# Optimization experiments

Measured on AMD Instinct MI355X. Metric: run time of the kernel, lower is better.

Reference implementation:

```python
import jax, jax.numpy as jnp
from jax import lax
import numpy as np

B, S, T, I, H, O = 128, 144, 50, 10, 64, 1


def setup_inputs() -> dict:
    key = jax.random.key(0)
    ks = jax.random.split(key, 11)
    sI = 1.0 / np.sqrt(H)
    x = jax.random.normal(ks[0], (B, S, T, I), dtype=jnp.float32)
    # PyTorch nn.GRU weights per direction: W_ih [3H,I], W_hh [3H,H], b_ih [3H], b_hh [3H]
    Wih_f = jax.random.normal(ks[1], (T, 3 * H, I), dtype=jnp.float32) * sI
    Whh_f = jax.random.normal(ks[2], (T, 3 * H, H), dtype=jnp.float32) * sI
    bih_f = jax.random.normal(ks[3], (T, 3 * H), dtype=jnp.float32) * sI
    bhh_f = jax.random.normal(ks[4], (T, 3 * H), dtype=jnp.float32) * sI
    Wih_b = jax.random.normal(ks[5], (T, 3 * H, I), dtype=jnp.float32) * sI
    Whh_b = jax.random.normal(ks[6], (T, 3 * H, H), dtype=jnp.float32) * sI
    bih_b = jax.random.normal(ks[7], (T, 3 * H), dtype=jnp.float32) * sI
    bhh_b = jax.random.normal(ks[8], (T, 3 * H), dtype=jnp.float32) * sI
    Wfc = jax.random.normal(ks[9], (T, O, 2 * H), dtype=jnp.float32) * sI
    bfc = jax.random.normal(ks[10], (T, O), dtype=jnp.float32) * sI
    return {"x": x, "Wih_f": Wih_f, "Whh_f": Whh_f, "bih_f": bih_f, "bhh_f": bhh_f,
            "Wih_b": Wih_b, "Whh_b": Whh_b, "bih_b": bih_b, "bhh_b": bhh_b,
            "Wfc": Wfc, "bfc": bfc}


def _gru_cell(x_t, h, Wih, Whh, bih, bhh):
    # PyTorch GRU cell math
    gi = x_t @ Wih.T + bih          # [B, 3H]
    gh = h @ Whh.T + bhh            # [B, 3H]
    i_r, i_z, i_n = jnp.split(gi, 3, axis=-1)
    h_r, h_z, h_n = jnp.split(gh, 3, axis=-1)
    r = jax.nn.sigmoid(i_r + h_r)
    z = jax.nn.sigmoid(i_z + h_z)
    n = jnp.tanh(i_n + r * h_n)
    return (1.0 - z) * n + z * h


def _per_turbine(xt, wih_f, whh_f, bih_f, bhh_f, wih_b, whh_b, bih_b, bhh_b, wfc, bfc):
    # xt: [B, S, I]
    x_sbi = jnp.transpose(xt, (1, 0, 2))  # [S, B, I]
    h0 = jnp.zeros((xt.shape[0], H), xt.dtype)

    def step(h, x_t):
        h = _gru_cell(x_t, h, wih_f, whh_f, bih_f, bhh_f)
        return h, None

    hf, _ = lax.scan(step, h0, x_sbi)  # forward final hidden = fwd output at t=S-1
    # backward-direction output at last timestep = first step of the reverse scan
    hb = _gru_cell(xt[:, -1, :], h0, wih_b, whh_b, bih_b, bhh_b)
    h = jnp.concatenate([hf, hb], axis=-1)  # [B, 2H]; dropout is identity at inference
    return h @ wfc.T + bfc  # [B, O]


def reference(x, Wih_f, Whh_f, bih_f, bhh_f, Wih_b, Whh_b, bih_b, bhh_b, Wfc, bfc):
    x_tbsi = jnp.transpose(x, (2, 0, 1, 3))  # [T, B, S, I]
    out = jax.vmap(_per_turbine)(x_tbsi, Wih_f, Whh_f, bih_f, bhh_f,
                                 Wih_b, Whh_b, bih_b, bhh_b, Wfc, bfc)  # [T, B, O]
    return jnp.transpose(out, (1, 2, 0))  # [B, O, T]
```

## Files before the change

kernel.cpp:

```cpp
#include <hip/hip_runtime.h>


typedef _Float16 f16;
typedef _Float16 f16x8 __attribute__((ext_vector_type(8)));
typedef float    f32x4 __attribute__((ext_vector_type(4)));

constexpr int B_N = 128, S_N = 144, T_N = 50, I_N = 10, H_N = 64, G3 = 192;
constexpr int BT16 = 16, NB16 = B_N / BT16;
constexpr int HST = 88;
constexpr float L2E = 1.44269504089f;

#define MFMA16(a, b, c) __builtin_amdgcn_mfma_f32_16x16x32_f16((a), (b), (c), 0, 0, 0)

__device__ __forceinline__ float fsig(float v) {
    return __builtin_amdgcn_rcpf(1.0f + __builtin_amdgcn_exp2f(-L2E * v));
}
__device__ __forceinline__ float ftanh(float v) {
    return 1.0f - 2.0f * __builtin_amdgcn_rcpf(1.0f + __builtin_amdgcn_exp2f(2.0f * L2E * v));
}

__global__ __launch_bounds__(256)
void pack_x(const float* __restrict__ x, f16* __restrict__ xP) {
    const int idx = blockIdx.x * 256 + threadIdx.x;
    if (idx >= B_N * S_N * T_N) return;
    const float* s = x + (size_t)idx * I_N;
    f16x8 lo, hi;
    #pragma unroll
    for (int e = 0; e < 8; ++e) lo[e] = (f16)s[e];
    hi[0] = (f16)s[8]; hi[1] = (f16)s[9]; hi[2] = (f16)1.0f;
    #pragma unroll
    for (int e = 3; e < 8; ++e) hi[e] = (f16)0.0f;
    f16* d = xP + (size_t)idx * 16;
    *(f16x8*)d = lo; *(f16x8*)(d + 8) = hi;
}

#define STEPP(ss, xf)                                                             \
    {                                                                             \
        const int cur = (ss) & 1, nxt = cur ^ 1;                                  \
        const f16x8 xA = xf;                                                      \
        if ((ss) + 2 < S_N && lg < 2)                                             \
            xf = *(const f16x8*)(xProw + (size_t)((ss) + 2) * (T_N * 16) + lg * 8); \
        const f16* hrow = &hL[tile][cur][lc][0];                                  \
        const f16x8 hA0 = *(const f16x8*)(hrow + lg * 8);                         \
        const f16x8 hA1 = *(const f16x8*)(hrow + 32 + lg * 8);                    \
        f32x4 aR  = {0,0,0,0}, aZ = {0,0,0,0}, aNH = {0,0,0,0}, aNX = {0,0,0,0};  \
        aR  = MFMA16(xA,  BxR,  aR);                                              \
        aZ  = MFMA16(xA,  BxZ,  aZ);                                              \
        aNX = MFMA16(xA,  BxN,  aNX);                                             \
        aR  = MFMA16(hA0, BhR0, aR);                                              \
        aR  = MFMA16(hA1, BhR1, aR);                                              \
        aZ  = MFMA16(hA0, BhZ0, aZ);                                              \
        aZ  = MFMA16(hA1, BhZ1, aZ);                                              \
        aNH = MFMA16(hA0, BhN0, aNH);                                             \
        aNH = MFMA16(hA1, BhN1, aNH);                                             \
        const int r0 = lg * 4;                                                    \
        _Pragma("unroll")                                                         \
        for (int j = 0; j < 4; ++j) {                                             \
            const float eA = __builtin_amdgcn_exp2f(aR[j]);                       \
            const float rr = __builtin_amdgcn_rcpf(1.0f + eA);                    \
            const float eB = __builtin_amdgcn_exp2f(aZ[j]);                       \
            const float eC = __builtin_amdgcn_exp2f(fmaf(rr, aNH[j] + bnhs, aNX[j])); \
            const float v  = 1.0f + eC;                                           \
            const float ip = __builtin_amdgcn_rcpf(v * (1.0f + eB));              \
            const float p  = (eC - 1.0f) * eB;                                    \
            ho[j] = fmaf(ho[j], v, p) * ip;                                       \
            hL[tile][nxt][r0 + j][uc + lc] = (f16)ho[j];                          \
        }                                                                         \
        asm volatile("s_waitcnt lgkmcnt(0)" ::: "memory");                        \
        __builtin_amdgcn_s_barrier();                                             \
        asm volatile("" ::: "memory");                                            \
    }

__global__ __launch_bounds__(512, 1)
void gru_pair(const f16* __restrict__ xP, const float* __restrict__ x,
              const float* __restrict__ Wih_f, const float* __restrict__ Whh_f,
              const float* __restrict__ bih_f, const float* __restrict__ bhh_f,
              const float* __restrict__ Wih_b, const float* __restrict__ bih_b,
              const float* __restrict__ bhh_b,
              const float* __restrict__ Wfc,   const float* __restrict__ bfc,
              float* __restrict__ out)
{
    __shared__ f16   hL[2][2][BT16][HST];
    __shared__ float hfL[2 * BT16][H_N + 1];
    __shared__ float hbL[2 * BT16][H_N + 1];

    const int tid  = threadIdx.x;
    const int w    = tid >> 6, l = tid & 63;
    const int tile = w >> 2;
    const int uc   = (w & 3) * 16;
    const int lc   = l & 15;
    const int lg   = l >> 4;
    const int t    = blockIdx.x >> 2;
    const int b0   = (blockIdx.x & 3) * 32 + tile * 16;

    {
        f16* hp = &hL[0][0][0][0];
        for (int i = tid; i < 2 * 2 * BT16 * HST; i += 512) hp[i] = (f16)0.0f;
    }

    const float* Whh = Whh_f + (size_t)t * G3 * H_N;
    const float* Wih = Wih_f + (size_t)t * G3 * I_N;
    const f16* xProw = xP + ((size_t)(b0 + lc) * S_N * T_N + t) * 16;

    const float sRZ = -L2E, sN = 2.0f * L2E;
    auto loadBh = [&](int g, int kk, float sc) -> f16x8 {
        const float4* p = (const float4*)(Whh + (size_t)g * H_N + kk * 32 + lg * 8);
        const float4 a = p[0], b = p[1];
        f16x8 v;
        v[0] = (f16)(sc * a.x); v[1] = (f16)(sc * a.y); v[2] = (f16)(sc * a.z); v[3] = (f16)(sc * a.w);
        v[4] = (f16)(sc * b.x); v[5] = (f16)(sc * b.y); v[6] = (f16)(sc * b.z); v[7] = (f16)(sc * b.w);
        return v;
    };
    auto loadBx = [&](int g, bool rz, float sc) -> f16x8 {
        f16x8 v;
        #pragma unroll
        for (int j = 0; j < 8; ++j) {
            const int k = lg * 8 + j;
            float val = 0.0f;
            if (k < I_N)       val = Wih[(size_t)g * I_N + k];
            else if (k == 10)  val = bih_f[t * G3 + g] + (rz ? bhh_f[t * G3 + g] : 0.0f);
            v[j] = (f16)(sc * val);
        }
        return v;
    };

    const f16x8 BhR0 = loadBh(uc + lc, 0, sRZ),        BhR1 = loadBh(uc + lc, 1, sRZ);
    const f16x8 BhZ0 = loadBh(64 + uc + lc, 0, sRZ),   BhZ1 = loadBh(64 + uc + lc, 1, sRZ);
    const f16x8 BhN0 = loadBh(128 + uc + lc, 0, sN),   BhN1 = loadBh(128 + uc + lc, 1, sN);
    const f16x8 BxR  = loadBx(uc + lc, true, sRZ);
    const f16x8 BxZ  = loadBx(64 + uc + lc, true, sRZ);
    const f16x8 BxN  = loadBx(128 + uc + lc, false, sN);
    const float bnhs = sN * bhh_f[t * G3 + 128 + uc + lc];

    f16x8 xsA, xsB;
    #pragma unroll
    for (int e = 0; e < 8; ++e) { xsA[e] = (f16)0.0f; xsB[e] = (f16)0.0f; }
    if (lg < 2) {
        xsA = *(const f16x8*)(xProw + lg * 8);
        xsB = *(const f16x8*)(xProw + (size_t)(T_N * 16) + lg * 8);
    }

    float ho[4] = {0.f, 0.f, 0.f, 0.f};

    __syncthreads();

    for (int s = 0; s < S_N; s += 2) {
        STEPP(s,     xsA)
        STEPP(s + 1, xsB)
    }

    {
        const int r0 = lg * 4;
        #pragma unroll
        for (int j = 0; j < 4; ++j) hfL[tile * BT16 + r0 + j][uc + lc] = ho[j];
    }

    {
        const int row2 = tid >> 4;
        const int j0   = (tid & 15) * 4;
        const int bq   = (blockIdx.x & 3) * 32;
        const float* wib = Wih_b + (size_t)t * G3 * I_N;
        const float* bib = bih_b + t * G3;
        const float* bhb = bhh_b + t * G3;
        float2 xr[5];
        const float2* xp2 = (const float2*)(x + (((size_t)(bq + row2) * S_N + (S_N - 1)) * T_N + t) * I_N);
        #pragma unroll
        for (int k = 0; k < 5; ++k) xr[k] = xp2[k];
        #pragma unroll
        for (int m = 0; m < 4; ++m) {
            const int j = j0 + m;
            float ir = bib[j], iz = bib[64 + j], inn = bib[128 + j];
            const float2* wr = (const float2*)(wib + (size_t)j * I_N);
            const float2* wz = (const float2*)(wib + (size_t)(64 + j) * I_N);
            const float2* wn = (const float2*)(wib + (size_t)(128 + j) * I_N);
            #pragma unroll
            for (int k = 0; k < 5; ++k) {
                ir  = fmaf(wr[k].x, xr[k].x, fmaf(wr[k].y, xr[k].y, ir));
                iz  = fmaf(wz[k].x, xr[k].x, fmaf(wz[k].y, xr[k].y, iz));
                inn = fmaf(wn[k].x, xr[k].x, fmaf(wn[k].y, xr[k].y, inn));
            }
            const float r  = fsig(ir + bhb[j]);
            const float z  = fsig(iz + bhb[64 + j]);
            const float nn = ftanh(inn + r * bhb[128 + j]);
            hbL[row2][j] = (1.0f - z) * nn;
        }
    }
    __syncthreads();

    if (tid < 2 * BT16) {
        const int bq = (blockIdx.x & 3) * 32;
        const float* wfc = Wfc + (size_t)t * 2 * H_N;
        float acc = bfc[t];
        #pragma unroll 4
        for (int j = 0; j < H_N; ++j) acc += hfL[tid][j] * wfc[j];
        #pragma unroll 4
        for (int j = 0; j < H_N; ++j) acc += hbL[tid][j] * wfc[64 + j];
        out[(size_t)(bq + tid) * T_N + t] = acc;
    }
}


#define LOADX_R(ss, q0, q1, q2, q3, q4)                                           \
    if ((ss) < S_N) {                                                             \
        const float* _p = x + (((size_t)(b0 + lc) * S_N + (ss)) * T_N + t) * I_N; \
        if (lg == 0) {                                                            \
            q0 = *(const float2*)(_p);     q1 = *(const float2*)(_p + 2);         \
            q2 = *(const float2*)(_p + 4); q3 = *(const float2*)(_p + 6);         \
        } else if (lg == 1) {                                                     \
            q4 = *(const float2*)(_p + 8);                                        \
        }                                                                         \
    }

#define STEP1(ss, q0, q1, q2, q3, q4)                                             \
    {                                                                             \
        const int cur = (ss) & 1, nxt = cur ^ 1;                                  \
        const f16* hrow = &hL[cur][lc][0];                                        \
        const f16x8 hA0 = *(const f16x8*)(hrow + lg * 8);                         \
        const f16x8 hA1 = *(const f16x8*)(hrow + 32 + lg * 8);                    \
        f16x8 xA;                                                                 \
        _Pragma("unroll")                                                         \
        for (int e = 0; e < 8; ++e) xA[e] = (f16)0.0f;                            \
        if (lg == 0) {                                                            \
            xA[0] = (f16)q0.x; xA[1] = (f16)q0.y; xA[2] = (f16)q1.x; xA[3] = (f16)q1.y; \
            xA[4] = (f16)q2.x; xA[5] = (f16)q2.y; xA[6] = (f16)q3.x; xA[7] = (f16)q3.y; \
        } else if (lg == 1) {                                                     \
            xA[0] = (f16)q4.x; xA[1] = (f16)q4.y; xA[2] = (f16)1.0f;              \
        }                                                                         \
        LOADX_R((ss) + 2, q0, q1, q2, q3, q4)                                     \
        f32x4 aR  = {0,0,0,0}, aZ = {0,0,0,0}, aNH = {0,0,0,0}, aNX = {0,0,0,0};  \
        aR  = MFMA16(xA,  BxR,  aR);                                              \
        aZ  = MFMA16(xA,  BxZ,  aZ);                                              \
        aNX = MFMA16(xA,  BxN,  aNX);                                             \
        aR  = MFMA16(hA0, BhR0, aR);                                              \
        aR  = MFMA16(hA1, BhR1, aR);                                              \
        aZ  = MFMA16(hA0, BhZ0, aZ);                                              \
        aZ  = MFMA16(hA1, BhZ1, aZ);                                              \
        aNH = MFMA16(hA0, BhN0, aNH);                                             \
        aNH = MFMA16(hA1, BhN1, aNH);                                             \
        const int r0 = lg * 4;                                                    \
        _Pragma("unroll")                                                         \
        for (int j = 0; j < 4; ++j) {                                             \
            const float rr = __builtin_amdgcn_rcpf(1.0f + __builtin_amdgcn_exp2f(aR[j])); \
            const float zz = __builtin_amdgcn_rcpf(1.0f + __builtin_amdgcn_exp2f(aZ[j])); \
            const float qq = __builtin_amdgcn_rcpf(1.0f + __builtin_amdgcn_exp2f(fmaf(rr, aNH[j] + bnhs, aNX[j]))); \
            const float nn = fmaf(-2.0f, qq, 1.0f);                               \
            ho[j] = fmaf(zz, ho[j] - nn, nn);                                     \
            hL[nxt][r0 + j][uc + lc] = (f16)ho[j];                                \
        }                                                                         \
        asm volatile("s_waitcnt lgkmcnt(0)" ::: "memory");                        \
        __builtin_amdgcn_s_barrier();                                             \
        asm volatile("" ::: "memory");                                            \
    }

__global__ __launch_bounds__(256, 2)
void gru_mfma1(const float* __restrict__ x,
               const float* __restrict__ Wih_f, const float* __restrict__ Whh_f,
               const float* __restrict__ bih_f, const float* __restrict__ bhh_f,
               const float* __restrict__ Wih_b, const float* __restrict__ bih_b,
               const float* __restrict__ bhh_b,
               const float* __restrict__ Wfc,   const float* __restrict__ bfc,
               float* __restrict__ out)
{
    __shared__ f16   hL[2][BT16][HST];
    __shared__ float hfL[BT16][H_N + 1];
    __shared__ float hbL[BT16][H_N + 1];

    const int tid = threadIdx.x;
    const int w   = tid >> 6, l = tid & 63;
    const int uc  = w * 16;
    const int lc  = l & 15;
    const int lg  = l >> 4;
    const int t   = blockIdx.x / NB16;
    const int b0  = (blockIdx.x % NB16) * BT16;

    {
        f16* hp = &hL[0][0][0];
        for (int i = tid; i < 2 * BT16 * HST; i += 256) hp[i] = (f16)0.0f;
    }

    const float* Whh = Whh_f + (size_t)t * G3 * H_N;
    const float* Wih = Wih_f + (size_t)t * G3 * I_N;

    const float sRZ = -L2E, sN = 2.0f * L2E;
    auto loadBh = [&](int g, int kk, float sc) -> f16x8 {
        const float4* p = (const float4*)(Whh + (size_t)g * H_N + kk * 32 + lg * 8);
        const float4 a = p[0], b = p[1];
        f16x8 v;
        v[0] = (f16)(sc * a.x); v[1] = (f16)(sc * a.y); v[2] = (f16)(sc * a.z); v[3] = (f16)(sc * a.w);
        v[4] = (f16)(sc * b.x); v[5] = (f16)(sc * b.y); v[6] = (f16)(sc * b.z); v[7] = (f16)(sc * b.w);
        return v;
    };
    auto loadBx = [&](int g, bool rz, float sc) -> f16x8 {
        f16x8 v;
        #pragma unroll
        for (int j = 0; j < 8; ++j) {
            const int k = lg * 8 + j;
            float val = 0.0f;
            if (k < I_N)       val = Wih[(size_t)g * I_N + k];
            else if (k == 10)  val = bih_f[t * G3 + g] + (rz ? bhh_f[t * G3 + g] : 0.0f);
            v[j] = (f16)(sc * val);
        }
        return v;
    };

    const f16x8 BhR0 = loadBh(uc + lc, 0, sRZ),        BhR1 = loadBh(uc + lc, 1, sRZ);
    const f16x8 BhZ0 = loadBh(64 + uc + lc, 0, sRZ),   BhZ1 = loadBh(64 + uc + lc, 1, sRZ);
    const f16x8 BhN0 = loadBh(128 + uc + lc, 0, sN),   BhN1 = loadBh(128 + uc + lc, 1, sN);
    const f16x8 BxR  = loadBx(uc + lc, true, sRZ);
    const f16x8 BxZ  = loadBx(64 + uc + lc, true, sRZ);
    const f16x8 BxN  = loadBx(128 + uc + lc, false, sN);
    const float bnhs = sN * bhh_f[t * G3 + 128 + uc + lc];

    float2 ra0 = {0.f,0.f}, ra1 = {0.f,0.f}, ra2 = {0.f,0.f}, ra3 = {0.f,0.f}, ra4 = {0.f,0.f};
    float2 rb0 = {0.f,0.f}, rb1 = {0.f,0.f}, rb2 = {0.f,0.f}, rb3 = {0.f,0.f}, rb4 = {0.f,0.f};
    LOADX_R(0, ra0, ra1, ra2, ra3, ra4)
    LOADX_R(1, rb0, rb1, rb2, rb3, rb4)

    float ho[4] = {0.f, 0.f, 0.f, 0.f};

    __syncthreads();

    for (int s = 0; s < S_N; s += 2) {
        STEP1(s,     ra0, ra1, ra2, ra3, ra4)
        STEP1(s + 1, rb0, rb1, rb2, rb3, rb4)
    }

    {
        const int r0 = lg * 4;
        #pragma unroll
        for (int j = 0; j < 4; ++j) hfL[r0 + j][uc + lc] = ho[j];
    }

    {
        const int row2 = tid >> 4;
        const int j0   = (tid & 15) * 4;
        const float* wib = Wih_b + (size_t)t * G3 * I_N;
        const float* bib = bih_b + t * G3;
        const float* bhb = bhh_b + t * G3;
        float xr[I_N];
        #pragma unroll
        for (int k = 0; k < I_N; ++k)
            xr[k] = x[(((size_t)(b0 + row2) * S_N + (S_N - 1)) * T_N + t) * I_N + k];
        #pragma unroll
        for (int m = 0; m < 4; ++m) {
            const int j = j0 + m;
            float ir = bib[j], iz = bib[64 + j], inn = bib[128 + j];
            #pragma unroll
            for (int k = 0; k < I_N; ++k) {
                const float xv = xr[k];
                ir  += wib[(size_t)j * I_N + k]          * xv;
                iz  += wib[(size_t)(64 + j) * I_N + k]   * xv;
                inn += wib[(size_t)(128 + j) * I_N + k]  * xv;
            }
            const float r  = fsig(ir + bhb[j]);
            const float z  = fsig(iz + bhb[64 + j]);
            const float nn = ftanh(inn + r * bhb[128 + j]);
            hbL[row2][j] = (1.0f - z) * nn;
        }
    }
    __syncthreads();

    if (tid < BT16) {
        const float* wfc = Wfc + (size_t)t * 2 * H_N;
        float acc = bfc[t];
        #pragma unroll 4
        for (int j = 0; j < H_N; ++j) acc += hfL[tid][j] * wfc[j];
        #pragma unroll 4
        for (int j = 0; j < H_N; ++j) acc += hbL[tid][j] * wfc[64 + j];
        out[(size_t)(b0 + tid) * T_N + t] = acc;
    }
}

extern "C" void kernel_launch(void* const* d_in, const int* in_sizes, int n_in,
                              void* d_out, int out_size, void* d_ws, size_t ws_size,
                              hipStream_t stream) {
    const float* x     = (const float*)d_in[0];
    const float* Wih_f = (const float*)d_in[1];
    const float* Whh_f = (const float*)d_in[2];
    const float* bih_f = (const float*)d_in[3];
    const float* bhh_f = (const float*)d_in[4];
    const float* Wih_b = (const float*)d_in[5];
    const float* bih_b = (const float*)d_in[7];
    const float* bhh_b = (const float*)d_in[8];
    const float* Wfc   = (const float*)d_in[9];
    const float* bfc   = (const float*)d_in[10];
    float* out = (float*)d_out;

    const size_t xp_bytes = (size_t)B_N * S_N * T_N * 16 * sizeof(f16);

    if (ws_size >= xp_bytes) {
        f16* xP = (f16*)d_ws;
        const int n = B_N * S_N * T_N;
        hipLaunchKernelGGL(pack_x, dim3((n + 255) / 256), dim3(256), 0, stream, x, xP);
        hipLaunchKernelGGL(gru_pair, dim3(T_N * 4), dim3(512), 0, stream,
                           xP, x, Wih_f, Whh_f, bih_f, bhh_f, Wih_b, bih_b, bhh_b, Wfc, bfc, out);
    } else {
        hipLaunchKernelGGL(gru_mfma1, dim3(T_N * NB16), dim3(256), 0, stream,
                           x, Wih_f, Whh_f, bih_f, bhh_f, Wih_b, bih_b, bhh_b, Wfc, bfc, out);
    }
}
```

Baseline: 101.9 us.

## Precompute next step's input-gate MFMAs off the recurrent critical path

Moves the x·Wih MFMAs for step s+1 to after the gate math of step s, so each recurrent step only runs the h·Whh MFMAs on its dependent chain. The h-projection accumulation is also split into two independent MFMA chains that are summed afterwards, which shortens the serial dependency. The cost is extra accumulator registers and a few vector adds. Correctness depends on the double-buffered x registers being swapped in the right order.

```diff
diff --git a/kernel.cpp b/kernel.cpp
--- a/kernel.cpp
+++ b/kernel.cpp
@@ -34,45 +34,48 @@
     *(f16x8*)d = lo; *(f16x8*)(d + 8) = hi;
 }
 
-#define STEPP(ss, xf)                                                             \
+#define STEPP(ss, useF, refillF, aXRc, aXZc, aXNc, aXRn, aXZn, aXNn)              \
     {                                                                             \
         const int cur = (ss) & 1, nxt = cur ^ 1;                                  \
-        const f16x8 xA = xf;                                                      \
-        if ((ss) + 2 < S_N && lg < 2)                                             \
-            xf = *(const f16x8*)(xProw + (size_t)((ss) + 2) * (T_N * 16) + lg * 8); \
         const f16* hrow = &hL[tile][cur][lc][0];                                  \
         const f16x8 hA0 = *(const f16x8*)(hrow + lg * 8);                         \
         const f16x8 hA1 = *(const f16x8*)(hrow + 32 + lg * 8);                    \
-        f32x4 aR  = {0,0,0,0}, aZ = {0,0,0,0}, aNH = {0,0,0,0}, aNX = {0,0,0,0};  \
-        aR  = MFMA16(xA,  BxR,  aR);                                              \
-        aZ  = MFMA16(xA,  BxZ,  aZ);                                              \
-        aNX = MFMA16(xA,  BxN,  aNX);                                             \
-        aR  = MFMA16(hA0, BhR0, aR);                                              \
-        aR  = MFMA16(hA1, BhR1, aR);                                              \
-        aZ  = MFMA16(hA0, BhZ0, aZ);                                              \
-        aZ  = MFMA16(hA1, BhZ1, aZ);                                              \
-        aNH = MFMA16(hA0, BhN0, aNH);                                             \
-        aNH = MFMA16(hA1, BhN1, aNH);                                             \
+        const f32x4 zv = {0.f, 0.f, 0.f, 0.f};                                    \
+        const f32x4 aRa = MFMA16(hA0, BhR0, aXRc);                                \
+        const f32x4 aRb = MFMA16(hA1, BhR1, zv);                                  \
+        const f32x4 aZa = MFMA16(hA0, BhZ0, aXZc);                                \
+        const f32x4 aZb = MFMA16(hA1, BhZ1, zv);                                  \
+        const f32x4 aNa = MFMA16(hA0, BhN0, zv);                                  \
+        const f32x4 aNb = MFMA16(hA1, BhN1, zv);                                  \
+        const f32x4 aR  = aRa + aRb;                                              \
+        const f32x4 aZ  = aZa + aZb;                                              \
+        const f32x4 aNH = aNa + aNb;                                              \
         const int r0 = lg * 4;                                                    \
         _Pragma("unroll")                                                         \
         for (int j = 0; j < 4; ++j) {                                             \
             const float eA = __builtin_amdgcn_exp2f(aR[j]);                       \
             const float rr = __builtin_amdgcn_rcpf(1.0f + eA);                    \
             const float eB = __builtin_amdgcn_exp2f(aZ[j]);                       \
-            const float eC = __builtin_amdgcn_exp2f(fmaf(rr, aNH[j] + bnhs, aNX[j])); \
+            const float eC = __builtin_amdgcn_exp2f(fmaf(rr, aNH[j] + bnhs, aXNc[j])); \
             const float v  = 1.0f + eC;                                           \
             const float ip = __builtin_amdgcn_rcpf(v * (1.0f + eB));              \
             const float p  = (eC - 1.0f) * eB;                                    \
             ho[j] = fmaf(ho[j], v, p) * ip;                                       \
             hL[tile][nxt][r0 + j][uc + lc] = (f16)ho[j];                          \
         }                                                                         \
+           \
+        aXRn = MFMA16(useF, BxR, zv);                                             \
+        aXZn = MFMA16(useF, BxZ, zv);                                             \
+        aXNn = MFMA16(useF, BxN, zv);                                             \
+        if ((ss) + 2 < S_N && lg < 2)                                             \
+            refillF = *(const f16x8*)(xProw + (size_t)((ss) + 2) * (T_N * 16) + lg * 8); \
         asm volatile("s_waitcnt lgkmcnt(0)" ::: "memory");                        \
         __builtin_amdgcn_s_barrier();                                             \
         asm volatile("" ::: "memory");                                            \
     }
 
 __global__ __launch_bounds__(512, 1)
-void gru_pair(const f16* __restrict__ xP, const float* __restrict__ x,
+void gru_pipe(const f16* __restrict__ xP, const float* __restrict__ x,
               const float* __restrict__ Wih_f, const float* __restrict__ Whh_f,
               const float* __restrict__ bih_f, const float* __restrict__ bhh_f,
               const float* __restrict__ Wih_b, const float* __restrict__ bih_b,
@@ -140,13 +143,22 @@
         xsB = *(const f16x8*)(xProw + (size_t)(T_N * 16) + lg * 8);
     }
 
+    f32x4 aXRA, aXZA, aXNA, aXRB, aXZB, aXNB;
+    {
+        const f32x4 zv = {0.f, 0.f, 0.f, 0.f};
+        aXRA = MFMA16(xsA, BxR, zv);
+        aXZA = MFMA16(xsA, BxZ, zv);
+        aXNA = MFMA16(xsA, BxN, zv);
+        aXRB = zv; aXZB = zv; aXNB = zv;
+    }
+
     float ho[4] = {0.f, 0.f, 0.f, 0.f};
 
     __syncthreads();
 
     for (int s = 0; s < S_N; s += 2) {
-        STEPP(s,     xsA)
-        STEPP(s + 1, xsB)
+        STEPP(s,     xsB, xsA, aXRA, aXZA, aXNA, aXRB, aXZB, aXNB)
+        STEPP(s + 1, xsA, xsB, aXRB, aXZB, aXNB, aXRA, aXZA, aXNA)
     }
 
     {
@@ -392,7 +404,7 @@
         f16* xP = (f16*)d_ws;
         const int n = B_N * S_N * T_N;
         hipLaunchKernelGGL(pack_x, dim3((n + 255) / 256), dim3(256), 0, stream, x, xP);
-        hipLaunchKernelGGL(gru_pair, dim3(T_N * 4), dim3(512), 0, stream,
+        hipLaunchKernelGGL(gru_pipe, dim3(T_N * 4), dim3(512), 0, stream,
                            xP, x, Wih_f, Whh_f, bih_f, bhh_f, Wih_b, bih_b, bhh_b, Wfc, bfc, out);
     } else {
         hipLaunchKernelGGL(gru_mfma1, dim3(T_N * NB16), dim3(256), 0, stream,
```

New measurement: 104.6 us. 1.03x slower.
